# Optimization experiments

Measured on AMD Instinct MI355X. Metric: run time of the kernel, lower is better.

Reference implementation:

```python
import jax, jax.numpy as jnp
import numpy as np

NEG = -1e9  # finite stand-in for -inf (keeps gradients NaN-free)
BLANK_LOGPROB = -1.0


def _lse(*xs):
    m = xs[0]
    for x in xs[1:]:
        m = jnp.maximum(m, x)
    s = sum(jnp.exp(x - m) for x in xs)
    return m + jnp.log(s)


def _forward_sum_loss(attn_logprob, text_lens, mel_lens):
    # attn_logprob: [B, 1, T, U]; text/mel lens: [B] int
    B, _, T, U = attn_logprob.shape
    x = attn_logprob[:, 0]                                   # [B, T, U]
    # pad a blank column at text index 0 (F.pad(..., (1,0,...)), value=blank_logprob)
    x = jnp.pad(x, ((0, 0), (0, 0), (1, 0)), constant_values=BLANK_LOGPROB)  # [B,T,U+1]
    # per-sample log_softmax over only the first text_len+1 columns (matches the
    # torch slice [:, :, :text_len+1] before LogSoftmax) -> mask padding columns
    cols = jnp.arange(U + 1)
    valid_col = cols[None, :] <= text_lens[:, None]          # [B, U+1]
    x = jnp.where(valid_col[:, None, :], x, NEG)
    lp = jax.nn.log_softmax(x, axis=-1)                      # [B, T, U+1]

    # CTC forward-sum. Target for sample b is [1, 2, ..., text_len_b] (all
    # distinct labels), extended with blanks: s=0..2U, label(s)=0 if s even else (s+1)//2.
    S = 2 * U + 1
    s = jnp.arange(S)
    lab = jnp.where(s % 2 == 0, 0, (s + 1) // 2)             # [S]
    odd = (s % 2 == 1)
    lp_ext = lp[:, :, lab]                                   # [B, T, S]
    # columns beyond text_len are NEG after log_softmax, so invalid label
    # positions (odd s with (s+1)//2 > text_len) are automatically killed.

    idx_last = 2 * text_lens                                 # [B] final blank position
    neg1 = jnp.full((B, 1), NEG, lp.dtype)
    neg2 = jnp.full((B, 2), NEG, lp.dtype)

    def step(alpha, lp_t):
        a1 = alpha                                           # stay
        a2 = jnp.concatenate([neg1, alpha[:, :-1]], axis=1)  # advance 1
        a3 = jnp.concatenate([neg2, alpha[:, :-2]], axis=1)  # skip (labels distinct)
        a3 = jnp.where(odd[None, :], a3, NEG)                # skip only into label positions
        new = lp_t + _lse(a1, a2, a3)                        # [B, S]
        fin = _lse(jnp.take_along_axis(new, idx_last[:, None], axis=1)[:, 0],
                   jnp.take_along_axis(new, (idx_last - 1)[:, None], axis=1)[:, 0])
        return new, fin

    alpha0 = jnp.full((B, S), NEG, lp.dtype).at[:, 0].set(0.0)
    lp_ts = jnp.transpose(lp_ext, (1, 0, 2))                 # [T, B, S]
    _, fins = jax.lax.scan(step, alpha0, lp_ts)              # [T, B]
    final = jnp.take_along_axis(fins, (mel_lens - 1)[None, :], axis=0)[0]  # [B]
    # nn.CTCLoss(reduction='mean') on a batch of 1 divides by target length;
    # zero_infinity zeroes out impossible alignments.
    loss = jnp.where(final < NEG / 2, 0.0, -final / text_lens.astype(lp.dtype))
    return jnp.mean(loss)


def setup_inputs() -> dict:
    key = jax.random.key(0)
    k1, k2, k3 = jax.random.split(key, 3)
    B, T, U = 64, 1000, 250
    attn_logprob = jax.random.normal(k1, (B, 1, T, U), dtype=jnp.float32)
    text_lens = jax.random.randint(k2, (B,), 50, U + 1, dtype=jnp.int32)
    mel_lens = jax.random.randint(k3, (B,), 600, T + 1, dtype=jnp.int32)
    return {"attn_logprob": attn_logprob, "text_lens": text_lens, "mel_lens": mel_lens}


def reference(attn_logprob, text_lens, mel_lens):
    return _forward_sum_loss(attn_logprob, text_lens, mel_lens)
```

## Files before the change

### kernel.cpp

```cpp
#include <hip/hip_runtime.h>

#define NEGF -1000000000.0f
#define LOG2E 1.4426950408889634f
#define LN2 0.6931471805599453f

constexpr int Bn = 64;
constexpr int Tn = 1000;
constexpr int Un = 250;

__device__ __forceinline__ float exp2fast(float x) { return __builtin_amdgcn_exp2f(x); }
__device__ __forceinline__ float log2fast(float x) { return __builtin_amdgcn_logf(x); }

template <int CTRL>
__device__ __forceinline__ float dppmov(float x) {
    return __int_as_float(__builtin_amdgcn_update_dpp(
        0, __float_as_int(x), CTRL, 0xf, 0xf, true));
}
__device__ __forceinline__ float dpp_wave_shr1(float x) { return dppmov<0x138>(x); }

__device__ __forceinline__ float wave_red_max(float x) {
    x = fmaxf(x, dppmov<0x111>(x));
    x = fmaxf(x, dppmov<0x112>(x));
    x = fmaxf(x, dppmov<0x114>(x));
    x = fmaxf(x, dppmov<0x118>(x));
    x = fmaxf(x, dppmov<0x142>(x));
    x = fmaxf(x, dppmov<0x143>(x));
    return __int_as_float(__builtin_amdgcn_readlane(__float_as_int(x), 63));
}
__device__ __forceinline__ float wave_red_sum(float x) {
    x += dppmov<0x111>(x);
    x += dppmov<0x112>(x);
    x += dppmov<0x114>(x);
    x += dppmov<0x118>(x);
    x += dppmov<0x142>(x);
    x += dppmov<0x143>(x);
    return __int_as_float(__builtin_amdgcn_readlane(__float_as_int(x), 63));
}

__global__ void __launch_bounds__(256) zrow_kernel(const float* __restrict__ attn,
                                                   const int* __restrict__ text_lens,
                                                   float* __restrict__ Z2,
                                                   float* __restrict__ out) {
    if (blockIdx.x == 0 && threadIdx.x == 0) *out = 0.0f;
    int wid = threadIdx.x >> 6;
    int lane = threadIdx.x & 63;
    int row0 = (blockIdx.x * 4 + wid) * 4;

    float v[4][4];
    int Ls[4];
#pragma unroll
    for (int r = 0; r < 4; ++r) {
        int row = row0 + r;
        Ls[r] = text_lens[row / Tn];
        const float* p = attn + (size_t)row * Un;
#pragma unroll
        for (int i = 0; i < 4; ++i) {
            int u = lane + 64 * i;
            v[r][i] = (u < Un) ? p[u] : 0.0f;
        }
    }
#pragma unroll
    for (int r = 0; r < 4; ++r) {
        int L = Ls[r];
        float m = (lane == 0) ? -LOG2E : NEGF;
#pragma unroll
        for (int i = 0; i < 4; ++i) {
            int u = lane + 64 * i;
            v[r][i] = (u < L) ? v[r][i] * LOG2E : NEGF;
            m = fmaxf(m, v[r][i]);
        }
        m = wave_red_max(m);
        float s = (lane == 0) ? exp2fast(-LOG2E - m) : 0.0f;
#pragma unroll
        for (int i = 0; i < 4; ++i) s += exp2fast(v[r][i] - m);
        s = wave_red_sum(s);
        if (lane == 0) Z2[row0 + r] = m + log2fast(s);
    }
}

typedef float v2f __attribute__((ext_vector_type(2)));

#define CTC_REFILL(J, T)                                                      \
    {                                                                         \
        int tl_ = (T) <= last ? (T) : last;                                   \
        const char* rowp_ = pbase + (size_t)tl_ * 1000;                       \
        asm volatile("global_load_dwordx2 %0, %1, %2"                         \
                     : "=v"(lo[J]) : "v"(voff_lo), "s"(rowp_));               \
        asm volatile("global_load_dwordx2 %0, %1, %2"                         \
                     : "=v"(hi[J]) : "v"(voff_hi), "s"(rowp_));               \
    }

#define QGEN(Q, S, WCNT)                                                      \
    {                                                                         \
        asm volatile("s_waitcnt vmcnt(" #WCNT ")"                             \
                     : "+v"(lo[S]), "+v"(hi[S]));                             \
        qa[Q] = exp2fast(__builtin_fmaf(lo[S].x, LOG2E, bias0));              \
        qb[Q] = exp2fast(__builtin_fmaf(lo[S].y, LOG2E, bias1));              \
        qc[Q] = exp2fast(__builtin_fmaf(hi[S].x, LOG2E, bias2));              \
        qd[Q] = exp2fast(__builtin_fmaf(hi[S].y, LOG2E, bias3));              \
    }

#define STEP_Q(Q)                                                             \
    {                                                                         \
        float q0 = qa[Q], q1 = qb[Q], q2 = qc[Q], q3 = qd[Q];                 \
        float p7 = dpp_wave_shr1(a7);       \
        float s65 = a6 + a5, s43 = a4 + a3, s21 = a2 + a1, s0p = a0 + p7;     \
        a7 = (a7 + s65) * q3;  a6 = s65 * QB;                                 \
        a5 = (a5 + s43) * q2;  a4 = s43 * QB;                                 \
        a3 = (a3 + s21) * q1;  a2 = s21 * QB;                                 \
        a1 = (a1 + s0p) * q0;  a0 = s0p * QB;                                 \
    }

#define RENORM()                                                              \
    {                                                                         \
        float mx = fmaxf(fmaxf(fmaxf(a0, a1), fmaxf(a2, a3)),                 \
                         fmaxf(fmaxf(a4, a5), fmaxf(a6, a7)));                \
        mx = wave_red_max(mx);                \
        int e_ = (int)((__float_as_uint(mx) >> 23) & 255) - 127;              \
        float scale_ = __uint_as_float((unsigned)(127 - e_) << 23);           \
        a0 *= scale_; a1 *= scale_; a2 *= scale_; a3 *= scale_;               \
        a4 *= scale_; a5 *= scale_; a6 *= scale_; a7 *= scale_;               \
        Esum += (float)e_;                                                    \
    }

__global__ void __launch_bounds__(64, 1) ctc_kernel(const float* __restrict__ attn,
                                                    const int* __restrict__ text_lens,
                                                    const int* __restrict__ mel_lens,
                                                    const float* __restrict__ Z2,
                                                    float* __restrict__ out) {
    int b = blockIdx.x;
    int lane = threadIdx.x;
    int L = text_lens[b];
    int n_t = mel_lens[b];
    const char* pbase = (const char*)(attn + (size_t)b * Tn * Un);

    int voff_lo = lane * 16, voff_hi = lane * 16 + 8;
    if (lane == 62) { voff_lo = 992; voff_hi = 992; }
    if (lane == 63) { voff_lo = 0;   voff_hi = 0;   }
    int c0 = lane * 4;
    float bias0 = (c0 + 0 < L) ? 0.0f : -1000000.0f;
    float bias1 = (c0 + 1 < L) ? 0.0f : -1000000.0f;
    float bias2 = (c0 + 2 < L) ? 0.0f : -1000000.0f;
    float bias3 = (c0 + 3 < L) ? 0.0f : -1000000.0f;

    const float QB = 0.36787944117144233f;
    float a0 = (lane == 0) ? 1.0f : 0.0f;
    float a1 = 0.0f, a2 = 0.0f, a3 = 0.0f, a4 = 0.0f, a5 = 0.0f, a6 = 0.0f, a7 = 0.0f;
    float Esum = 0.0f;

    v2f lo[16], hi[16];
    float qa[8], qb[8], qc[8], qd[8];
    int last = n_t - 1;

#pragma unroll
    for (int j = 0; j < 16; ++j) CTC_REFILL(j, j);
    QGEN(0, 0, 30); QGEN(1, 1, 28); QGEN(2, 2, 26); QGEN(3, 3, 24);
    QGEN(4, 4, 22); QGEN(5, 5, 20); QGEN(6, 6, 18); QGEN(7, 7, 16);
#pragma unroll
    for (int j = 0; j < 8; ++j) CTC_REFILL(j, 16 + j);

    int full = n_t & ~15;
    int t = 0;
    for (; t < full; t += 16) {
        STEP_Q(0); QGEN(0, 8, 30);  CTC_REFILL(8,  t + 24);
        STEP_Q(1); QGEN(1, 9, 30);  CTC_REFILL(9,  t + 25);
        STEP_Q(2); QGEN(2, 10, 30); CTC_REFILL(10, t + 26);
        STEP_Q(3); QGEN(3, 11, 30); CTC_REFILL(11, t + 27);
        STEP_Q(4); QGEN(4, 12, 30); CTC_REFILL(12, t + 28);
        STEP_Q(5); QGEN(5, 13, 30); CTC_REFILL(13, t + 29);
        STEP_Q(6); QGEN(6, 14, 30); CTC_REFILL(14, t + 30);
        STEP_Q(7); QGEN(7, 15, 30); CTC_REFILL(15, t + 31);
        RENORM();
        STEP_Q(0); QGEN(0, 0, 30);  CTC_REFILL(0, t + 32);
        STEP_Q(1); QGEN(1, 1, 30);  CTC_REFILL(1, t + 33);
        STEP_Q(2); QGEN(2, 2, 30);  CTC_REFILL(2, t + 34);
        STEP_Q(3); QGEN(3, 3, 30);  CTC_REFILL(3, t + 35);
        STEP_Q(4); QGEN(4, 4, 30);  CTC_REFILL(4, t + 36);
        STEP_Q(5); QGEN(5, 5, 30);  CTC_REFILL(5, t + 37);
        STEP_Q(6); QGEN(6, 6, 30);  CTC_REFILL(6, t + 38);
        STEP_Q(7); QGEN(7, 7, 30);  CTC_REFILL(7, t + 39);
        RENORM();
    }
    if (t + 0 < n_t) STEP_Q(0);
    if (t + 1 < n_t) STEP_Q(1);
    if (t + 2 < n_t) STEP_Q(2);
    if (t + 3 < n_t) STEP_Q(3);
    if (t + 4 < n_t) STEP_Q(4);
    if (t + 5 < n_t) STEP_Q(5);
    if (t + 6 < n_t) STEP_Q(6);
    if (t + 7 < n_t) STEP_Q(7);
    if (t + 8 < n_t)  { RENORM(); QGEN(0, 8, 0); STEP_Q(0); }
    if (t + 9 < n_t)  { QGEN(1, 9, 0);  STEP_Q(1); }
    if (t + 10 < n_t) { QGEN(2, 10, 0); STEP_Q(2); }
    if (t + 11 < n_t) { QGEN(3, 11, 0); STEP_Q(3); }
    if (t + 12 < n_t) { QGEN(4, 12, 0); STEP_Q(4); }
    if (t + 13 < n_t) { QGEN(5, 13, 0); STEP_Q(5); }
    if (t + 14 < n_t) { QGEN(6, 14, 0); STEP_Q(6); }
    asm volatile("s_waitcnt vmcnt(0)" ::: "memory");

    __shared__ float sal[512];
    sal[lane * 8 + 0] = a0;
    sal[lane * 8 + 1] = a1;
    sal[lane * 8 + 2] = a2;
    sal[lane * 8 + 3] = a3;
    sal[lane * 8 + 4] = a4;
    sal[lane * 8 + 5] = a5;
    sal[lane * 8 + 6] = a6;
    sal[lane * 8 + 7] = a7;
    __syncthreads();

    float zs = 0.0f;
    for (int i = lane; i < n_t; i += 64) zs += Z2[b * Tn + i];
    zs = wave_red_sum(zs);

    if (lane == 0) {
        float ssum = sal[2 * L] + sal[2 * L - 1];
        float fin = (log2fast(ssum) + Esum - zs) * LN2;
        float loss = (ssum <= 0.0f) ? 0.0f : (-fin / (float)L);
        atomicAdd(out, loss * (1.0f / (float)Bn));
    }
}

extern "C" void kernel_launch(void* const* d_in, const int* in_sizes, int n_in,
                              void* d_out, int out_size, void* d_ws, size_t ws_size,
                              hipStream_t stream) {
    const float* attn = (const float*)d_in[0];
    const int* text_lens = (const int*)d_in[1];
    const int* mel_lens = (const int*)d_in[2];
    float* out = (float*)d_out;
    float* Z2 = (float*)d_ws;

    zrow_kernel<<<Bn * Tn / 16, 256, 0, stream>>>(attn, text_lens, Z2, out);
    ctc_kernel<<<Bn, 64, 0, stream>>>(attn, text_lens, mel_lens, Z2, out);
}
```

Baseline: 172.0 us.

## Fuse row-normalizer and CTC kernels with a global completion counter

Merges the row log-sum-exp kernel and the CTC recurrence kernel into one launch. The first 64 blocks run the CTC recurrence and the remaining blocks compute the row normalizers. The CTC blocks spin on an atomic counter only at the end, when they need the normalizer sum. This lets the normalizer pass overlap with the long serial recurrence and removes one kernel boundary. In exchange it adds a memset of the counter, a spin-wait on global memory, and a change from launch_bounds(64,1) to 256 for the CTC code path.

```diff
diff --git a/kernel.cpp b/kernel.cpp
--- a/kernel.cpp
+++ b/kernel.cpp
@@ -7,6 +7,7 @@
 constexpr int Bn = 64;
 constexpr int Tn = 1000;
 constexpr int Un = 250;
+constexpr int NZROW = Bn * Tn / 16;
 
 __device__ __forceinline__ float exp2fast(float x) { return __builtin_amdgcn_exp2f(x); }
 __device__ __forceinline__ float log2fast(float x) { return __builtin_amdgcn_logf(x); }
@@ -37,47 +38,6 @@
     return __int_as_float(__builtin_amdgcn_readlane(__float_as_int(x), 63));
 }
 
-__global__ void __launch_bounds__(256) zrow_kernel(const float* __restrict__ attn,
-                                                   const int* __restrict__ text_lens,
-                                                   float* __restrict__ Z2,
-                                                   float* __restrict__ out) {
-    if (blockIdx.x == 0 && threadIdx.x == 0) *out = 0.0f;
-    int wid = threadIdx.x >> 6;
-    int lane = threadIdx.x & 63;
-    int row0 = (blockIdx.x * 4 + wid) * 4;
-
-    float v[4][4];
-    int Ls[4];
-#pragma unroll
-    for (int r = 0; r < 4; ++r) {
-        int row = row0 + r;
-        Ls[r] = text_lens[row / Tn];
-        const float* p = attn + (size_t)row * Un;
-#pragma unroll
-        for (int i = 0; i < 4; ++i) {
-            int u = lane + 64 * i;
-            v[r][i] = (u < Un) ? p[u] : 0.0f;
-        }
-    }
-#pragma unroll
-    for (int r = 0; r < 4; ++r) {
-        int L = Ls[r];
-        float m = (lane == 0) ? -LOG2E : NEGF;
-#pragma unroll
-        for (int i = 0; i < 4; ++i) {
-            int u = lane + 64 * i;
-            v[r][i] = (u < L) ? v[r][i] * LOG2E : NEGF;
-            m = fmaxf(m, v[r][i]);
-        }
-        m = wave_red_max(m);
-        float s = (lane == 0) ? exp2fast(-LOG2E - m) : 0.0f;
-#pragma unroll
-        for (int i = 0; i < 4; ++i) s += exp2fast(v[r][i] - m);
-        s = wave_red_sum(s);
-        if (lane == 0) Z2[row0 + r] = m + log2fast(s);
-    }
-}
-
 typedef float v2f __attribute__((ext_vector_type(2)));
 
 #define CTC_REFILL(J, T)                                                      \
@@ -123,11 +83,56 @@
         Esum += (float)e_;                                                    \
     }
 
-__global__ void __launch_bounds__(64, 1) ctc_kernel(const float* __restrict__ attn,
+__global__ void __launch_bounds__(256) fused_kernel(const float* __restrict__ attn,
                                                     const int* __restrict__ text_lens,
                                                     const int* __restrict__ mel_lens,
-                                                    const float* __restrict__ Z2,
+                                                    float* __restrict__ Z2,
+                                                    unsigned int* __restrict__ done,
                                                     float* __restrict__ out) {
+    if (blockIdx.x >= (unsigned)Bn) {
+        int bz = blockIdx.x - Bn;
+        if (bz == 0 && threadIdx.x == 0) *out = 0.0f;
+        int wid = threadIdx.x >> 6;
+        int lane = threadIdx.x & 63;
+        int row0 = (bz * 4 + wid) * 4;
+
+        float v[4][4];
+        int Ls[4];
+#pragma unroll
+        for (int r = 0; r < 4; ++r) {
+            int row = row0 + r;
+            Ls[r] = text_lens[row / Tn];
+            const float* p = attn + (size_t)row * Un;
+#pragma unroll
+            for (int i = 0; i < 4; ++i) {
+                int u = lane + 64 * i;
+                v[r][i] = (u < Un) ? p[u] : 0.0f;
+            }
+        }
+#pragma unroll
+        for (int r = 0; r < 4; ++r) {
+            int L = Ls[r];
+            float m = (lane == 0) ? -LOG2E : NEGF;
+#pragma unroll
+            for (int i = 0; i < 4; ++i) {
+                int u = lane + 64 * i;
+                v[r][i] = (u < L) ? v[r][i] * LOG2E : NEGF;
+                m = fmaxf(m, v[r][i]);
+            }
+            m = wave_red_max(m);
+            float s = (lane == 0) ? exp2fast(-LOG2E - m) : 0.0f;
+#pragma unroll
+            for (int i = 0; i < 4; ++i) s += exp2fast(v[r][i] - m);
+            s = wave_red_sum(s);
+            if (lane == 0) Z2[row0 + r] = m + log2fast(s);
+        }
+        __threadfence();
+        __syncthreads();
+        if (threadIdx.x == 0) atomicAdd(done, 1u);
+        return;
+    }
+
+    if (threadIdx.x >= 64) return;
     int b = blockIdx.x;
     int lane = threadIdx.x;
     int L = text_lens[b];
@@ -207,7 +212,12 @@
     sal[lane * 8 + 5] = a5;
     sal[lane * 8 + 6] = a6;
     sal[lane * 8 + 7] = a7;
-    __syncthreads();
+    asm volatile("s_waitcnt lgkmcnt(0)" ::: "memory");
+
+    while (__hip_atomic_load(done, __ATOMIC_ACQUIRE, __HIP_MEMORY_SCOPE_AGENT)
+           < (unsigned)NZROW) {
+        __builtin_amdgcn_s_sleep(32);
+    }
 
     float zs = 0.0f;
     for (int i = lane; i < n_t; i += 64) zs += Z2[b * Tn + i];
@@ -228,8 +238,11 @@
     const int* text_lens = (const int*)d_in[1];
     const int* mel_lens = (const int*)d_in[2];
     float* out = (float*)d_out;
-    float* Z2 = (float*)d_ws;
-
-    zrow_kernel<<<Bn * Tn / 16, 256, 0, stream>>>(attn, text_lens, Z2, out);
-    ctc_kernel<<<Bn, 64, 0, stream>>>(attn, text_lens, mel_lens, Z2, out);
-}
+
+    unsigned int* done = (unsigned int*)d_ws;
+    float* Z2 = (float*)((char*)d_ws + 1024);
+
+    hipMemsetAsync(d_ws, 0, 1024, stream);
+    fused_kernel<<<Bn + NZROW, 256, 0, stream>>>(attn, text_lens, mel_lens,
+                                                 Z2, done, out);
+}
```

Measured after the change: 495.2 us. 188% more time.

## Fuse softmax normalizer into CTC kernel via a second concurrent wavefront

Applied to the files above, without the earlier changes.

Drops the separate row log-sum-exp kernel and the Z2 workspace. Each CTC block now runs two wavefronts: one performs the alpha recursion, the other streams the same rows and accumulates the per-row log normalizer, and the two combine through shared memory. This removes one kernel launch and the second read of attn, and it only normalizes rows up to mel_len. The cost is an extra wavefront per block competing for the same SIMD, and a memset launch to zero the output.

```diff
diff --git a/kernel.cpp b/kernel.cpp
--- a/kernel.cpp
+++ b/kernel.cpp
@@ -37,47 +37,6 @@
     return __int_as_float(__builtin_amdgcn_readlane(__float_as_int(x), 63));
 }
 
-__global__ void __launch_bounds__(256) zrow_kernel(const float* __restrict__ attn,
-                                                   const int* __restrict__ text_lens,
-                                                   float* __restrict__ Z2,
-                                                   float* __restrict__ out) {
-    if (blockIdx.x == 0 && threadIdx.x == 0) *out = 0.0f;
-    int wid = threadIdx.x >> 6;
-    int lane = threadIdx.x & 63;
-    int row0 = (blockIdx.x * 4 + wid) * 4;
-
-    float v[4][4];
-    int Ls[4];
-#pragma unroll
-    for (int r = 0; r < 4; ++r) {
-        int row = row0 + r;
-        Ls[r] = text_lens[row / Tn];
-        const float* p = attn + (size_t)row * Un;
-#pragma unroll
-        for (int i = 0; i < 4; ++i) {
-            int u = lane + 64 * i;
-            v[r][i] = (u < Un) ? p[u] : 0.0f;
-        }
-    }
-#pragma unroll
-    for (int r = 0; r < 4; ++r) {
-        int L = Ls[r];
-        float m = (lane == 0) ? -LOG2E : NEGF;
-#pragma unroll
-        for (int i = 0; i < 4; ++i) {
-            int u = lane + 64 * i;
-            v[r][i] = (u < L) ? v[r][i] * LOG2E : NEGF;
-            m = fmaxf(m, v[r][i]);
-        }
-        m = wave_red_max(m);
-        float s = (lane == 0) ? exp2fast(-LOG2E - m) : 0.0f;
-#pragma unroll
-        for (int i = 0; i < 4; ++i) s += exp2fast(v[r][i] - m);
-        s = wave_red_sum(s);
-        if (lane == 0) Z2[row0 + r] = m + log2fast(s);
-    }
-}
-
 typedef float v2f __attribute__((ext_vector_type(2)));
 
 #define CTC_REFILL(J, T)                                                      \
@@ -123,13 +82,25 @@
         Esum += (float)e_;                                                    \
     }
 
-__global__ void __launch_bounds__(64, 1) ctc_kernel(const float* __restrict__ attn,
-                                                    const int* __restrict__ text_lens,
-                                                    const int* __restrict__ mel_lens,
-                                                    const float* __restrict__ Z2,
-                                                    float* __restrict__ out) {
+#define ZSTEP(J, WCNT)                                                        \
+    {                                                                         \
+        asm volatile("s_waitcnt vmcnt(" #WCNT ")"                             \
+                     : "+v"(lo[J]), "+v"(hi[J]));                             \
+        float q0 = exp2fast(__builtin_fmaf(lo[J].x, LOG2E, bias0));           \
+        float q1 = exp2fast(__builtin_fmaf(lo[J].y, LOG2E, bias1));           \
+        float q2 = exp2fast(__builtin_fmaf(hi[J].x, LOG2E, bias2));           \
+        float q3 = exp2fast(__builtin_fmaf(hi[J].y, LOG2E, bias3));           \
+        float rsum = wave_red_sum((q0 + q1) + (q2 + q3));                     \
+        zacc += log2fast(QB + rsum);                                          \
+    }
+
+__global__ void __launch_bounds__(128, 1) ctc_fused_kernel(
+        const float* __restrict__ attn,
+        const int* __restrict__ text_lens,
+        const int* __restrict__ mel_lens,
+        float* __restrict__ out) {
     int b = blockIdx.x;
-    int lane = threadIdx.x;
+    int lane = threadIdx.x & 63;
     int L = text_lens[b];
     int n_t = mel_lens[b];
     const char* pbase = (const char*)(attn + (size_t)b * Tn * Un);
@@ -144,76 +115,123 @@
     float bias3 = (c0 + 3 < L) ? 0.0f : -1000000.0f;
 
     const float QB = 0.36787944117144233f;
-    float a0 = (lane == 0) ? 1.0f : 0.0f;
-    float a1 = 0.0f, a2 = 0.0f, a3 = 0.0f, a4 = 0.0f, a5 = 0.0f, a6 = 0.0f, a7 = 0.0f;
     float Esum = 0.0f;
-
     v2f lo[16], hi[16];
-    float qa[8], qb[8], qc[8], qd[8];
     int last = n_t - 1;
 
+    __shared__ float sal[512];
+    __shared__ float salz;
+
+    if (threadIdx.x < 64) {
+        float a0 = (lane == 0) ? 1.0f : 0.0f;
+        float a1 = 0.0f, a2 = 0.0f, a3 = 0.0f, a4 = 0.0f, a5 = 0.0f,
+              a6 = 0.0f, a7 = 0.0f;
+        float qa[8], qb[8], qc[8], qd[8];
+
 #pragma unroll
-    for (int j = 0; j < 16; ++j) CTC_REFILL(j, j);
-    QGEN(0, 0, 30); QGEN(1, 1, 28); QGEN(2, 2, 26); QGEN(3, 3, 24);
-    QGEN(4, 4, 22); QGEN(5, 5, 20); QGEN(6, 6, 18); QGEN(7, 7, 16);
+        for (int j = 0; j < 16; ++j) CTC_REFILL(j, j);
+        QGEN(0, 0, 30); QGEN(1, 1, 28); QGEN(2, 2, 26); QGEN(3, 3, 24);
+        QGEN(4, 4, 22); QGEN(5, 5, 20); QGEN(6, 6, 18); QGEN(7, 7, 16);
 #pragma unroll
-    for (int j = 0; j < 8; ++j) CTC_REFILL(j, 16 + j);
-
-    int full = n_t & ~15;
-    int t = 0;
-    for (; t < full; t += 16) {
-        STEP_Q(0); QGEN(0, 8, 30);  CTC_REFILL(8,  t + 24);
-        STEP_Q(1); QGEN(1, 9, 30);  CTC_REFILL(9,  t + 25);
-        STEP_Q(2); QGEN(2, 10, 30); CTC_REFILL(10, t + 26);
-        STEP_Q(3); QGEN(3, 11, 30); CTC_REFILL(11, t + 27);
-        STEP_Q(4); QGEN(4, 12, 30); CTC_REFILL(12, t + 28);
-        STEP_Q(5); QGEN(5, 13, 30); CTC_REFILL(13, t + 29);
-        STEP_Q(6); QGEN(6, 14, 30); CTC_REFILL(14, t + 30);
-        STEP_Q(7); QGEN(7, 15, 30); CTC_REFILL(15, t + 31);
-        RENORM();
-        STEP_Q(0); QGEN(0, 0, 30);  CTC_REFILL(0, t + 32);
-        STEP_Q(1); QGEN(1, 1, 30);  CTC_REFILL(1, t + 33);
-        STEP_Q(2); QGEN(2, 2, 30);  CTC_REFILL(2, t + 34);
-        STEP_Q(3); QGEN(3, 3, 30);  CTC_REFILL(3, t + 35);
-        STEP_Q(4); QGEN(4, 4, 30);  CTC_REFILL(4, t + 36);
-        STEP_Q(5); QGEN(5, 5, 30);  CTC_REFILL(5, t + 37);
-        STEP_Q(6); QGEN(6, 6, 30);  CTC_REFILL(6, t + 38);
-        STEP_Q(7); QGEN(7, 7, 30);  CTC_REFILL(7, t + 39);
-        RENORM();
-    }
-    if (t + 0 < n_t) STEP_Q(0);
-    if (t + 1 < n_t) STEP_Q(1);
-    if (t + 2 < n_t) STEP_Q(2);
-    if (t + 3 < n_t) STEP_Q(3);
-    if (t + 4 < n_t) STEP_Q(4);
-    if (t + 5 < n_t) STEP_Q(5);
-    if (t + 6 < n_t) STEP_Q(6);
-    if (t + 7 < n_t) STEP_Q(7);
-    if (t + 8 < n_t)  { RENORM(); QGEN(0, 8, 0); STEP_Q(0); }
-    if (t + 9 < n_t)  { QGEN(1, 9, 0);  STEP_Q(1); }
-    if (t + 10 < n_t) { QGEN(2, 10, 0); STEP_Q(2); }
-    if (t + 11 < n_t) { QGEN(3, 11, 0); STEP_Q(3); }
-    if (t + 12 < n_t) { QGEN(4, 12, 0); STEP_Q(4); }
-    if (t + 13 < n_t) { QGEN(5, 13, 0); STEP_Q(5); }
-    if (t + 14 < n_t) { QGEN(6, 14, 0); STEP_Q(6); }
-    asm volatile("s_waitcnt vmcnt(0)" ::: "memory");
-
-    __shared__ float sal[512];
-    sal[lane * 8 + 0] = a0;
-    sal[lane * 8 + 1] = a1;
-    sal[lane * 8 + 2] = a2;
-    sal[lane * 8 + 3] = a3;
-    sal[lane * 8 + 4] = a4;
-    sal[lane * 8 + 5] = a5;
-    sal[lane * 8 + 6] = a6;
-    sal[lane * 8 + 7] = a7;
+        for (int j = 0; j < 8; ++j) CTC_REFILL(j, 16 + j);
+
+        int full = n_t & ~15;
+        int t = 0;
+        for (; t < full; t += 16) {
+            STEP_Q(0); QGEN(0, 8, 30);  CTC_REFILL(8,  t + 24);
+            STEP_Q(1); QGEN(1, 9, 30);  CTC_REFILL(9,  t + 25);
+            STEP_Q(2); QGEN(2, 10, 30); CTC_REFILL(10, t + 26);
+            STEP_Q(3); QGEN(3, 11, 30); CTC_REFILL(11, t + 27);
+            STEP_Q(4); QGEN(4, 12, 30); CTC_REFILL(12, t + 28);
+            STEP_Q(5); QGEN(5, 13, 30); CTC_REFILL(13, t + 29);
+            STEP_Q(6); QGEN(6, 14, 30); CTC_REFILL(14, t + 30);
+            STEP_Q(7); QGEN(7, 15, 30); CTC_REFILL(15, t + 31);
+            RENORM();
+            STEP_Q(0); QGEN(0, 0, 30);  CTC_REFILL(0, t + 32);
+            STEP_Q(1); QGEN(1, 1, 30);  CTC_REFILL(1, t + 33);
+            STEP_Q(2); QGEN(2, 2, 30);  CTC_REFILL(2, t + 34);
+            STEP_Q(3); QGEN(3, 3, 30);  CTC_REFILL(3, t + 35);
+            STEP_Q(4); QGEN(4, 4, 30);  CTC_REFILL(4, t + 36);
+            STEP_Q(5); QGEN(5, 5, 30);  CTC_REFILL(5, t + 37);
+            STEP_Q(6); QGEN(6, 6, 30);  CTC_REFILL(6, t + 38);
+            STEP_Q(7); QGEN(7, 7, 30);  CTC_REFILL(7, t + 39);
+            RENORM();
+        }
+        if (t + 0 < n_t) STEP_Q(0);
+        if (t + 1 < n_t) STEP_Q(1);
+        if (t + 2 < n_t) STEP_Q(2);
+        if (t + 3 < n_t) STEP_Q(3);
+        if (t + 4 < n_t) STEP_Q(4);
+        if (t + 5 < n_t) STEP_Q(5);
+        if (t + 6 < n_t) STEP_Q(6);
+        if (t + 7 < n_t) STEP_Q(7);
+        if (t + 8 < n_t)  { RENORM(); QGEN(0, 8, 0); STEP_Q(0); }
+        if (t + 9 < n_t)  { QGEN(1, 9, 0);  STEP_Q(1); }
+        if (t + 10 < n_t) { QGEN(2, 10, 0); STEP_Q(2); }
+        if (t + 11 < n_t) { QGEN(3, 11, 0); STEP_Q(3); }
+        if (t + 12 < n_t) { QGEN(4, 12, 0); STEP_Q(4); }
+        if (t + 13 < n_t) { QGEN(5, 13, 0); STEP_Q(5); }
+        if (t + 14 < n_t) { QGEN(6, 14, 0); STEP_Q(6); }
+        asm volatile("s_waitcnt vmcnt(0)" ::: "memory");
+
+        sal[lane * 8 + 0] = a0;
+        sal[lane * 8 + 1] = a1;
+        sal[lane * 8 + 2] = a2;
+        sal[lane * 8 + 3] = a3;
+        sal[lane * 8 + 4] = a4;
+        sal[lane * 8 + 5] = a5;
+        sal[lane * 8 + 6] = a6;
+        sal[lane * 8 + 7] = a7;
+    } else {
+        float zacc = 0.0f;
+
+#pragma unroll
+        for (int j = 0; j < 16; ++j) CTC_REFILL(j, j);
+
+        int full = n_t & ~15;
+        int t = 0;
+        for (; t < full; t += 16) {
+            ZSTEP(0, 30);  CTC_REFILL(0, t + 16);
+            ZSTEP(1, 30);  CTC_REFILL(1, t + 17);
+            ZSTEP(2, 30);  CTC_REFILL(2, t + 18);
+            ZSTEP(3, 30);  CTC_REFILL(3, t + 19);
+            ZSTEP(4, 30);  CTC_REFILL(4, t + 20);
+            ZSTEP(5, 30);  CTC_REFILL(5, t + 21);
+            ZSTEP(6, 30);  CTC_REFILL(6, t + 22);
+            ZSTEP(7, 30);  CTC_REFILL(7, t + 23);
+            ZSTEP(8, 30);  CTC_REFILL(8, t + 24);
+            ZSTEP(9, 30);  CTC_REFILL(9, t + 25);
+            ZSTEP(10, 30); CTC_REFILL(10, t + 26);
+            ZSTEP(11, 30); CTC_REFILL(11, t + 27);
+            ZSTEP(12, 30); CTC_REFILL(12, t + 28);
+            ZSTEP(13, 30); CTC_REFILL(13, t + 29);
+            ZSTEP(14, 30); CTC_REFILL(14, t + 30);
+            ZSTEP(15, 30); CTC_REFILL(15, t + 31);
+        }
+        if (t + 0 < n_t) ZSTEP(0, 0);
+        if (t + 1 < n_t) ZSTEP(1, 0);
+        if (t + 2 < n_t) ZSTEP(2, 0);
+        if (t + 3 < n_t) ZSTEP(3, 0);
+        if (t + 4 < n_t) ZSTEP(4, 0);
+        if (t + 5 < n_t) ZSTEP(5, 0);
+        if (t + 6 < n_t) ZSTEP(6, 0);
+        if (t + 7 < n_t) ZSTEP(7, 0);
+        if (t + 8 < n_t) ZSTEP(8, 0);
+        if (t + 9 < n_t) ZSTEP(9, 0);
+        if (t + 10 < n_t) ZSTEP(10, 0);
+        if (t + 11 < n_t) ZSTEP(11, 0);
+        if (t + 12 < n_t) ZSTEP(12, 0);
+        if (t + 13 < n_t) ZSTEP(13, 0);
+        if (t + 14 < n_t) ZSTEP(14, 0);
+        asm volatile("s_waitcnt vmcnt(0)" ::: "memory");
+
+        if (threadIdx.x == 64) salz = zacc;
+    }
+
     __syncthreads();
 
-    float zs = 0.0f;
-    for (int i = lane; i < n_t; i += 64) zs += Z2[b * Tn + i];
-    zs = wave_red_sum(zs);
-
-    if (lane == 0) {
+    if (threadIdx.x == 0) {
+        float zs = salz;
         float ssum = sal[2 * L] + sal[2 * L - 1];
         float fin = (log2fast(ssum) + Esum - zs) * LN2;
         float loss = (ssum <= 0.0f) ? 0.0f : (-fin / (float)L);
@@ -228,8 +246,7 @@
     const int* text_lens = (const int*)d_in[1];
     const int* mel_lens = (const int*)d_in[2];
     float* out = (float*)d_out;
-    float* Z2 = (float*)d_ws;
-
-    zrow_kernel<<<Bn * Tn / 16, 256, 0, stream>>>(attn, text_lens, Z2, out);
-    ctc_kernel<<<Bn, 64, 0, stream>>>(attn, text_lens, mel_lens, Z2, out);
-}
+
+    hipMemsetAsync(out, 0, sizeof(float), stream);
+    ctc_fused_kernel<<<Bn, 128, 0, stream>>>(attn, text_lens, mel_lens, out);
+}
```

After: 161.1 us. -6.3%, faster.
